# Kernel optimization log

Hardware: AMD Instinct MI355X
Metric: run time of the kernel (lower is better)

Reference implementation:

```python
import jax, jax.numpy as jnp
import numpy as np

N_HEAD = 12
NEG_INF = -1e30


def setup_inputs() -> dict:
    key = jax.random.key(0)
    ks = jax.random.split(key, 12)
    bs, q_len, c_len, d = 2, 2048, 2048, 768
    s = 1.0 / np.sqrt(d)
    return {
        "query": jax.random.normal(ks[0], (bs, q_len, d), jnp.float32),
        "context": jax.random.normal(ks[1], (bs, c_len, d), jnp.float32),
        "c_mask": jax.random.randint(ks[2], (bs, c_len), 0, 2, jnp.int32),
        "Wq_w": jax.random.normal(ks[3], (d, d), jnp.float32) * s,
        "Wq_b": jnp.zeros((d,), jnp.float32),
        "Wk_w": jax.random.normal(ks[4], (d, d), jnp.float32) * s,
        "Wk_b": jnp.zeros((d,), jnp.float32),
        "Wv_w": jax.random.normal(ks[5], (d, d), jnp.float32) * s,
        "Wv_b": jnp.zeros((d,), jnp.float32),
        "fc_w": jax.random.normal(ks[6], (d, d), jnp.float32) * s,
        "fc_b": jnp.zeros((d,), jnp.float32),
    }


def reference(query, context, c_mask, Wq_w, Wq_b, Wk_w, Wk_b, Wv_w, Wv_b, fc_w, fc_b):
    bs, q_len, d = query.shape
    c_len = context.shape[1]
    d_k = d // N_HEAD
    a = 1.0 / np.sqrt(d_k)

    # QKV projections (torch Linear: y = x @ W.T + b), split into heads
    q = (query @ Wq_w.T + Wq_b).reshape(bs, q_len, N_HEAD, d_k)
    k = (context @ Wk_w.T + Wk_b).reshape(bs, c_len, N_HEAD, d_k)
    v = (context @ Wv_w.T + Wv_b).reshape(bs, c_len, N_HEAD, d_k)

    # scores [bs, n_head, q_len, c_len]
    s = jnp.einsum('bqhd,bchd->bhqc', q, k) * a

    # mask_logits: s * m + (1 - m) * -1e30, mask broadcast over heads and q
    m = c_mask.astype(s.dtype)[:, None, None, :]
    s = s * m + (1.0 - m) * NEG_INF

    p = jax.nn.softmax(s, axis=-1)  # dropout p=0.0 -> identity

    out = jnp.einsum('bhqc,bchd->bqhd', p, v).reshape(bs, q_len, d)
    return out @ fc_w.T + fc_b
```

## Files before the change

kernel.cpp:

```cpp
#include <hip/hip_runtime.h>
#include <cstdint>

#define D_MODEL 768
#define NH      12
#define DKH     64
#define SEQ     2048
#define BS      2
#define MROWS   (BS*SEQ)

typedef __bf16 bf16x8 __attribute__((ext_vector_type(8)));
typedef float  f32x4  __attribute__((ext_vector_type(4)));
typedef unsigned int u32_as1 __attribute__((address_space(1)));
typedef unsigned int u32_as3 __attribute__((address_space(3)));

__device__ __forceinline__ void gld16(const void* g, void* l) {
  __builtin_amdgcn_global_load_lds((const u32_as1*)g, (u32_as3*)l, 16, 0, 0);
}
__device__ __forceinline__ unsigned short f2bf(float x) {
  return __builtin_bit_cast(unsigned short, (__bf16)x);
}

__global__ void cvt2(const float* __restrict__ a, const float* __restrict__ b,
                     unsigned short* __restrict__ oa, unsigned short* __restrict__ ob) {
  const float* in = blockIdx.y ? b : a;
  unsigned short* out = blockIdx.y ? ob : oa;
  int i = blockIdx.x * 256 + threadIdx.x;
  float4 v = reinterpret_cast<const float4*>(in)[i];
  ushort4 o; o.x = f2bf(v.x); o.y = f2bf(v.y); o.z = f2bf(v.z); o.w = f2bf(v.w);
  reinterpret_cast<ushort4*>(out)[i] = o;
}
__global__ void cvt4(const float* __restrict__ a, const float* __restrict__ b,
                     const float* __restrict__ c, const float* __restrict__ d,
                     unsigned short* __restrict__ oa, unsigned short* __restrict__ ob,
                     unsigned short* __restrict__ oc, unsigned short* __restrict__ od) {
  const float* in; unsigned short* out;
  switch (blockIdx.y) {
    case 0: in = a; out = oa; break;
    case 1: in = b; out = ob; break;
    case 2: in = c; out = oc; break;
    default: in = d; out = od; break;
  }
  int i = blockIdx.x * 256 + threadIdx.x;
  float4 v = reinterpret_cast<const float4*>(in)[i];
  ushort4 o; o.x = f2bf(v.x); o.y = f2bf(v.y); o.z = f2bf(v.z); o.w = f2bf(v.w);
  reinterpret_cast<ushort4*>(out)[i] = o;
}

template<bool OUT_F32>
__device__ __forceinline__ void gemm128_body(
    const unsigned short* __restrict__ A, const unsigned short* __restrict__ B,
    const float* __restrict__ bias, int biasRow, void* __restrict__ Cout,
    int ldc, int m0, int n0)
{
  __shared__ alignas(16) char sA[2][16384];
  __shared__ alignas(16) char sB[2][16384];
  const int tid = threadIdx.x;
  const int w = tid >> 6, l = tid & 63;
  const int g16 = l >> 4, c16 = l & 15;
  const int wr = (w >> 1) * 64, wc = (w & 1) * 64;

  auto stage = [&](const unsigned short* __restrict__ P, int p0, int kt, char* dst) {
#pragma unroll
    for (int i = 0; i < 4; i++) {
      int ch = w * 4 + i;
      int X = ch * 1024 + l * 16;
      int row = X >> 7;
      int sl = ((X >> 4) & 7) ^ (row & 7);
      gld16(P + (size_t)(p0 + row) * 768 + kt + sl * 8, dst + ch * 1024);
    }
  };

  f32x4 acc[4][4];
#pragma unroll
  for (int m = 0; m < 4; m++)
#pragma unroll
    for (int n = 0; n < 4; n++) acc[m][n] = f32x4{0.f, 0.f, 0.f, 0.f};

  stage(A, m0, 0, sA[0]);
  stage(B, n0, 0, sB[0]);
  __syncthreads();
  int cur = 0;
  for (int kt = 0; kt < 768; kt += 64) {
    if (kt + 64 < 768) {
      stage(A, m0, kt + 64, sA[cur ^ 1]);
      stage(B, n0, kt + 64, sB[cur ^ 1]);
    }
    __builtin_amdgcn_s_setprio(1);
#pragma unroll
    for (int kk = 0; kk < 2; kk++) {
      bf16x8 af[4], bq[4];
#pragma unroll
      for (int m = 0; m < 4; m++) {
        int row = wr + m * 16 + c16, slot = kk * 4 + g16;
        af[m] = *(const bf16x8*)(sA[cur] + row * 128 + ((slot ^ (row & 7)) << 4));
      }
#pragma unroll
      for (int n = 0; n < 4; n++) {
        int row = wc + n * 16 + c16, slot = kk * 4 + g16;
        bq[n] = *(const bf16x8*)(sB[cur] + row * 128 + ((slot ^ (row & 7)) << 4));
      }
#pragma unroll
      for (int m = 0; m < 4; m++)
#pragma unroll
        for (int n = 0; n < 4; n++)
          acc[m][n] = __builtin_amdgcn_mfma_f32_16x16x32_bf16(af[m], bq[n], acc[m][n], 0, 0, 0);
    }
    __builtin_amdgcn_s_setprio(0);
    __syncthreads();
    cur ^= 1;
  }

#pragma unroll
  for (int m = 0; m < 4; m++)
#pragma unroll
    for (int n = 0; n < 4; n++)
#pragma unroll
      for (int r = 0; r < 4; r++) {
        int row = m0 + wr + m * 16 + g16 * 4 + r;
        int col = n0 + wc + n * 16 + c16;
        float v = acc[m][n][r] + (biasRow ? bias[row] : bias[col]);
        if constexpr (OUT_F32) ((float*)Cout)[(size_t)row * ldc + col] = v;
        else ((unsigned short*)Cout)[(size_t)row * ldc + col] = f2bf(v);
      }
}

__global__ __launch_bounds__(256, 2) void gemm_qkv(
    const unsigned short* __restrict__ q_bf, const unsigned short* __restrict__ c_bf,
    const unsigned short* __restrict__ wq, const unsigned short* __restrict__ wk,
    const unsigned short* __restrict__ wv,
    const float* __restrict__ bq, const float* __restrict__ bk,
    const float* __restrict__ bv,
    unsigned short* __restrict__ Qb, unsigned short* __restrict__ Kb,
    unsigned short* __restrict__ Vtb)
{
  const int x = blockIdx.x;
  const int lin = (x & 7) * 24 + (x >> 3);
  const int tf = lin % 6, ts = lin / 6;
  const unsigned short *A, *B; const float* bias; unsigned short* C;
  int m0, n0, ldc, biasRow;
  switch (blockIdx.y) {
    case 0:  A = q_bf; B = wq;   bias = bq; C = Qb;  m0 = ts*128; n0 = tf*128; ldc = 768;  biasRow = 0; break;
    case 1:  A = c_bf; B = wk;   bias = bk; C = Kb;  m0 = ts*128; n0 = tf*128; ldc = 768;  biasRow = 0; break;
    default: A = wv;   B = c_bf; bias = bv; C = Vtb; m0 = tf*128; n0 = ts*128; ldc = 4096; biasRow = 1; break;
  }
  gemm128_body<false>(A, B, bias, biasRow, C, ldc, m0, n0);
}

__global__ __launch_bounds__(256, 2) void gemm_fc(
    const unsigned short* __restrict__ Ob, const unsigned short* __restrict__ wf,
    const float* __restrict__ fb, float* __restrict__ out)
{
  const int x = blockIdx.x;
  const int lin = (x & 7) * 24 + (x >> 3);
  const int tf = lin % 6, ts = lin / 6;
  gemm128_body<true>(Ob, wf, fb, 0, out, 768, ts * 128, tf * 128);
}

__global__ __launch_bounds__(256, 4) void attn_kernel(
    const unsigned short* __restrict__ Qb, const unsigned short* __restrict__ Kb,
    const unsigned short* __restrict__ Vt, const int* __restrict__ cmask,
    unsigned short* __restrict__ Ob)
{
  __shared__ alignas(16) char sK[2][8192];
  __shared__ alignas(16) char sV[2][8192];
  __shared__ alignas(16) char sP[8192];
  const int tid = threadIdx.x, w = tid >> 6, l = tid & 63;
  const int g16 = l >> 4, c16 = l & 15;
  const int flat = blockIdx.x;
  const int xcd = flat & 7, sidx = flat >> 3;
  const int p = xcd + 8 * (sidx >> 5);
  const int qt = sidx & 31;
  const int h = p % 12, b = p / 12;
  const int qrow0 = b * SEQ + qt * 64;
  const int crow0 = b * SEQ;

  bf16x8 qa[2];
  {
    const unsigned short* qp =
        Qb + (size_t)(qrow0 + w * 16 + c16) * D_MODEL + h * DKH + g16 * 8;
    qa[0] = *(const bf16x8*)(qp);
    qa[1] = *(const bf16x8*)(qp + 32);
  }

  auto stageK = [&](int ct, int buf) {
#pragma unroll
    for (int i = 0; i < 2; i++) {
      int ch = w * 2 + i;
      int X = ch * 1024 + l * 16;
      int row = X >> 7;
      int sl = ((X >> 4) & 7) ^ (row & 7);
      gld16(Kb + (size_t)(crow0 + ct + row) * D_MODEL + h * DKH + sl * 8,
            sK[buf] + ch * 1024);
    }
  };
  auto stageV = [&](int ct, int buf) {
#pragma unroll
    for (int i = 0; i < 2; i++) {
      int ch = w * 2 + i;
      int X = ch * 1024 + l * 16;
      int row = X >> 7;
      int sl = ((X >> 4) & 7) ^ (row & 7);
      gld16(Vt + (size_t)(h * DKH + row) * (size_t)MROWS + crow0 + ct + sl * 8,
            sV[buf] + ch * 1024);
    }
  };

  f32x4 accO[4], accL;
#pragma unroll
  for (int n = 0; n < 4; n++) accO[n] = f32x4{0.f, 0.f, 0.f, 0.f};
  accL = f32x4{0.f, 0.f, 0.f, 0.f};
  const __bf16 one = (__bf16)1.0f;
  const bf16x8 vones = {one, one, one, one, one, one, one, one};

  stageK(0, 0); stageV(0, 0);
  __syncthreads();
  int cur = 0;

  for (int ct = 0; ct < SEQ; ct += 64) {
    if (ct + 64 < SEQ) { stageK(ct + 64, cur ^ 1); stageV(ct + 64, cur ^ 1); }

    int mk[4];
#pragma unroll
    for (int n = 0; n < 4; n++) mk[n] = cmask[crow0 + ct + n * 16 + c16];

    f32x4 s[4];
#pragma unroll
    for (int n = 0; n < 4; n++) s[n] = f32x4{0.f, 0.f, 0.f, 0.f};
    __builtin_amdgcn_s_setprio(1);
#pragma unroll
    for (int kk = 0; kk < 2; kk++) {
      bf16x8 kf[4];
#pragma unroll
      for (int n = 0; n < 4; n++) {
        int row = n * 16 + c16, slot = kk * 4 + g16;
        kf[n] = *(const bf16x8*)(sK[cur] + row * 128 + ((slot ^ (row & 7)) << 4));
      }
#pragma unroll
      for (int n = 0; n < 4; n++)
        s[n] = __builtin_amdgcn_mfma_f32_16x16x32_bf16(qa[kk], kf[n], s[n], 0, 0, 0);
    }
    __builtin_amdgcn_s_setprio(0);

#pragma unroll
    for (int r = 0; r < 4; r++) {
      int prow = g16 * 4 + r;
#pragma unroll
      for (int n = 0; n < 4; n++) {
        float pv = mk[n] ? __expf(s[n][r] * 0.125f) : 0.f;
        int slot = n * 2 + (c16 >> 3);
        int addr = w * 2048 + prow * 128 + ((slot ^ (prow & 7)) << 4) + (c16 & 7) * 2;
        *(__bf16*)(sP + addr) = (__bf16)pv;
      }
    }

    __builtin_amdgcn_s_setprio(1);
#pragma unroll
    for (int kk = 0; kk < 2; kk++) {
      bf16x8 pa, vf[4];
      {
        int prow = c16, slot = kk * 4 + g16;
        pa = *(const bf16x8*)(sP + w * 2048 + prow * 128 + ((slot ^ (prow & 7)) << 4));
      }
#pragma unroll
      for (int n = 0; n < 4; n++) {
        int vrow = n * 16 + c16, slot = kk * 4 + g16;
        vf[n] = *(const bf16x8*)(sV[cur] + vrow * 128 + ((slot ^ (vrow & 7)) << 4));
      }
#pragma unroll
      for (int n = 0; n < 4; n++)
        accO[n] = __builtin_amdgcn_mfma_f32_16x16x32_bf16(pa, vf[n], accO[n], 0, 0, 0);
      accL = __builtin_amdgcn_mfma_f32_16x16x32_bf16(pa, vones, accL, 0, 0, 0);
    }
    __builtin_amdgcn_s_setprio(0);

    __syncthreads();
    cur ^= 1;
  }

#pragma unroll
  for (int r = 0; r < 4; r++) {
    float inv = 1.0f / accL[r];
#pragma unroll
    for (int n = 0; n < 4; n++) {
      int row = qrow0 + w * 16 + g16 * 4 + r;
      int col = h * DKH + n * 16 + c16;
      Ob[(size_t)row * D_MODEL + col] = f2bf(accO[n][r] * inv);
    }
  }
}

extern "C" void kernel_launch(void* const* d_in, const int* in_sizes, int n_in,
                              void* d_out, int out_size, void* d_ws, size_t ws_size,
                              hipStream_t stream) {
  const float* query   = (const float*)d_in[0];
  const float* context = (const float*)d_in[1];
  const int*   cmask   = (const int*)d_in[2];
  const float* Wq_w = (const float*)d_in[3];
  const float* Wq_b = (const float*)d_in[4];
  const float* Wk_w = (const float*)d_in[5];
  const float* Wk_b = (const float*)d_in[6];
  const float* Wv_w = (const float*)d_in[7];
  const float* Wv_b = (const float*)d_in[8];
  const float* fc_w = (const float*)d_in[9];
  const float* fc_b = (const float*)d_in[10];
  float* out = (float*)d_out;

  unsigned short* ws   = (unsigned short*)d_ws;
  const size_t NQ = (size_t)MROWS * D_MODEL;
  const size_t NW = (size_t)D_MODEL * D_MODEL;
  unsigned short* q_bf = ws;
  unsigned short* c_bf = q_bf + NQ;
  unsigned short* Qb   = c_bf + NQ;
  unsigned short* Kb   = Qb + NQ;
  unsigned short* Vtb  = Kb + NQ;
  unsigned short* Ob   = Vtb + NQ;
  unsigned short* wq   = Ob + NQ;
  unsigned short* wk   = wq + NW;
  unsigned short* wv   = wk + NW;
  unsigned short* wf   = wv + NW;

  cvt2<<<dim3(NQ / 4 / 256, 2), 256, 0, stream>>>(query, context, q_bf, c_bf);
  cvt4<<<dim3(NW / 4 / 256, 4), 256, 0, stream>>>(Wq_w, Wk_w, Wv_w, fc_w, wq, wk, wv, wf);

  gemm_qkv<<<dim3(192, 3), 256, 0, stream>>>(
      q_bf, c_bf, wq, wk, wv, Wq_b, Wk_b, Wv_b, Qb, Kb, Vtb);

  attn_kernel<<<768, 256, 0, stream>>>(Qb, Kb, Vtb, cmask, Ob);

  gemm_fc<<<192, 256, 0, stream>>>(Ob, wf, fc_b, out);
}
```

Measured before the change: 105.7 us.

## Split attention context range across two wave groups per block and reduce

The attention kernel now launches 512 threads per block, with two groups of four waves each covering half of the context length. Each group keeps its own K/V/P buffers, and the partial output and row-sum accumulators are combined through shared memory at the end. The aim is more waves in flight per query tile, since the softmax is unnormalised and partials can simply be added. In exchange the K/V double-buffered prefetch is gone: each iteration loads and then syncs before computing, so load latency is exposed and block-wide barriers now couple both groups.

```diff
diff --git a/kernel.cpp b/kernel.cpp
--- a/kernel.cpp
+++ b/kernel.cpp
@@ -156,15 +156,16 @@
   gemm128_body<true>(Ob, wf, fb, 0, out, 768, ts * 128, tf * 128);
 }
 
-__global__ __launch_bounds__(256, 4) void attn_kernel(
+__global__ __launch_bounds__(512, 6) void attn_kernel(
     const unsigned short* __restrict__ Qb, const unsigned short* __restrict__ Kb,
     const unsigned short* __restrict__ Vt, const int* __restrict__ cmask,
     unsigned short* __restrict__ Ob)
 {
   __shared__ alignas(16) char sK[2][8192];
   __shared__ alignas(16) char sV[2][8192];
-  __shared__ alignas(16) char sP[8192];
+  __shared__ alignas(16) char sP[2][8192];
   const int tid = threadIdx.x, w = tid >> 6, l = tid & 63;
+  const int wl = w & 3, grp = w >> 2;
   const int g16 = l >> 4, c16 = l & 15;
   const int flat = blockIdx.x;
   const int xcd = flat & 7, sidx = flat >> 3;
@@ -172,36 +173,36 @@
   const int qt = sidx & 31;
   const int h = p % 12, b = p / 12;
   const int qrow0 = b * SEQ + qt * 64;
-  const int crow0 = b * SEQ;
+  const int cbase = b * SEQ + grp * 1024;
 
   bf16x8 qa[2];
   {
     const unsigned short* qp =
-        Qb + (size_t)(qrow0 + w * 16 + c16) * D_MODEL + h * DKH + g16 * 8;
+        Qb + (size_t)(qrow0 + wl * 16 + c16) * D_MODEL + h * DKH + g16 * 8;
     qa[0] = *(const bf16x8*)(qp);
     qa[1] = *(const bf16x8*)(qp + 32);
   }
 
-  auto stageK = [&](int ct, int buf) {
+  auto stageK = [&](int cg) {
 #pragma unroll
     for (int i = 0; i < 2; i++) {
-      int ch = w * 2 + i;
+      int ch = wl * 2 + i;
       int X = ch * 1024 + l * 16;
       int row = X >> 7;
       int sl = ((X >> 4) & 7) ^ (row & 7);
-      gld16(Kb + (size_t)(crow0 + ct + row) * D_MODEL + h * DKH + sl * 8,
-            sK[buf] + ch * 1024);
+      gld16(Kb + (size_t)(cg + row) * D_MODEL + h * DKH + sl * 8,
+            sK[grp] + ch * 1024);
     }
   };
-  auto stageV = [&](int ct, int buf) {
+  auto stageV = [&](int cg) {
 #pragma unroll
     for (int i = 0; i < 2; i++) {
-      int ch = w * 2 + i;
+      int ch = wl * 2 + i;
       int X = ch * 1024 + l * 16;
       int row = X >> 7;
       int sl = ((X >> 4) & 7) ^ (row & 7);
-      gld16(Vt + (size_t)(h * DKH + row) * (size_t)MROWS + crow0 + ct + sl * 8,
-            sV[buf] + ch * 1024);
+      gld16(Vt + (size_t)(h * DKH + row) * (size_t)MROWS + cg + sl * 8,
+            sV[grp] + ch * 1024);
     }
   };
 
@@ -212,16 +213,13 @@
   const __bf16 one = (__bf16)1.0f;
   const bf16x8 vones = {one, one, one, one, one, one, one, one};
 
-  stageK(0, 0); stageV(0, 0);
-  __syncthreads();
-  int cur = 0;
-
-  for (int ct = 0; ct < SEQ; ct += 64) {
-    if (ct + 64 < SEQ) { stageK(ct + 64, cur ^ 1); stageV(ct + 64, cur ^ 1); }
+  for (int ct = 0; ct < 1024; ct += 64) {
+    stageK(cbase + ct); stageV(cbase + ct);
+    __syncthreads();
 
     int mk[4];
 #pragma unroll
-    for (int n = 0; n < 4; n++) mk[n] = cmask[crow0 + ct + n * 16 + c16];
+    for (int n = 0; n < 4; n++) mk[n] = cmask[cbase + ct + n * 16 + c16];
 
     f32x4 s[4];
 #pragma unroll
@@ -233,7 +231,7 @@
 #pragma unroll
       for (int n = 0; n < 4; n++) {
         int row = n * 16 + c16, slot = kk * 4 + g16;
-        kf[n] = *(const bf16x8*)(sK[cur] + row * 128 + ((slot ^ (row & 7)) << 4));
+        kf[n] = *(const bf16x8*)(sK[grp] + row * 128 + ((slot ^ (row & 7)) << 4));
       }
 #pragma unroll
       for (int n = 0; n < 4; n++)
@@ -248,8 +246,8 @@
       for (int n = 0; n < 4; n++) {
         float pv = mk[n] ? __expf(s[n][r] * 0.125f) : 0.f;
         int slot = n * 2 + (c16 >> 3);
-        int addr = w * 2048 + prow * 128 + ((slot ^ (prow & 7)) << 4) + (c16 & 7) * 2;
-        *(__bf16*)(sP + addr) = (__bf16)pv;
+        int addr = wl * 2048 + prow * 128 + ((slot ^ (prow & 7)) << 4) + (c16 & 7) * 2;
+        *(__bf16*)(sP[grp] + addr) = (__bf16)pv;
       }
     }
 
@@ -259,12 +257,12 @@
       bf16x8 pa, vf[4];
       {
         int prow = c16, slot = kk * 4 + g16;
-        pa = *(const bf16x8*)(sP + w * 2048 + prow * 128 + ((slot ^ (prow & 7)) << 4));
+        pa = *(const bf16x8*)(sP[grp] + wl * 2048 + prow * 128 + ((slot ^ (prow & 7)) << 4));
       }
 #pragma unroll
       for (int n = 0; n < 4; n++) {
         int vrow = n * 16 + c16, slot = kk * 4 + g16;
-        vf[n] = *(const bf16x8*)(sV[cur] + vrow * 128 + ((slot ^ (vrow & 7)) << 4));
+        vf[n] = *(const bf16x8*)(sV[grp] + vrow * 128 + ((slot ^ (vrow & 7)) << 4));
       }
 #pragma unroll
       for (int n = 0; n < 4; n++)
@@ -274,17 +272,37 @@
     __builtin_amdgcn_s_setprio(0);
 
     __syncthreads();
-    cur ^= 1;
-  }
-
-#pragma unroll
-  for (int r = 0; r < 4; r++) {
-    float inv = 1.0f / accL[r];
-#pragma unroll
-    for (int n = 0; n < 4; n++) {
-      int row = qrow0 + w * 16 + g16 * 4 + r;
-      int col = h * DKH + n * 16 + c16;
-      Ob[(size_t)row * D_MODEL + col] = f2bf(accO[n][r] * inv);
+  }
+
+  {
+    float* oArea = (float*)&sK[0][0];
+    float* lArea = (float*)&sV[0][0];
+    const int slot = wl * 64 + l;
+    if (grp == 1) {
+#pragma unroll
+      for (int n = 0; n < 4; n++)
+        *reinterpret_cast<f32x4*>(&oArea[slot * 16 + n * 4]) = accO[n];
+      *reinterpret_cast<f32x4*>(&lArea[slot * 4]) = accL;
+    }
+    __syncthreads();
+    if (grp == 0) {
+#pragma unroll
+      for (int n = 0; n < 4; n++) {
+        f32x4 o1 = *reinterpret_cast<const f32x4*>(&oArea[slot * 16 + n * 4]);
+#pragma unroll
+        for (int r = 0; r < 4; r++) accO[n][r] += o1[r];
+      }
+      f32x4 l1 = *reinterpret_cast<const f32x4*>(&lArea[slot * 4]);
+#pragma unroll
+      for (int r = 0; r < 4; r++) {
+        float inv = 1.0f / (accL[r] + l1[r]);
+#pragma unroll
+        for (int n = 0; n < 4; n++) {
+          int row = qrow0 + wl * 16 + g16 * 4 + r;
+          int col = h * DKH + n * 16 + c16;
+          Ob[(size_t)row * D_MODEL + col] = f2bf(accO[n][r] * inv);
+        }
+      }
     }
   }
 }
@@ -325,7 +343,7 @@
   gemm_qkv<<<dim3(192, 3), 256, 0, stream>>>(
       q_bf, c_bf, wq, wk, wv, Wq_b, Wk_b, Wv_b, Qb, Kb, Vtb);
 
-  attn_kernel<<<768, 256, 0, stream>>>(Qb, Kb, Vtb, cmask, Ob);
+  attn_kernel<<<768, 512, 0, stream>>>(Qb, Kb, Vtb, cmask, Ob);
 
   gemm_fc<<<192, 256, 0, stream>>>(Ob, wf, fc_b, out);
 }
```

Result: slower. 122.2 us (+15.6%).
